# Performance work log

Hardware: AMD Instinct MI355X
Metric: run time of the kernel (lower is better)

## Reference

```python
import jax, jax.numpy as jnp
import numpy as np

B, C, H, W = 2, 256, 64, 64
HEADS, DIM_HEAD = 8, 64
INNER = HEADS * DIM_HEAD


def setup_inputs() -> dict:
    key = jax.random.key(0)
    k1, k2, k3, k4 = jax.random.split(key, 4)
    x = jax.random.normal(k1, (B, C, H, W), dtype=jnp.float32)
    # 1x1 conv weights stored as [out_ch, in_ch]
    w_qkv = jax.random.normal(k2, (3 * INNER, C), dtype=jnp.float32) * (1.0 / np.sqrt(C))
    w_out = jax.random.normal(k3, (C, INNER), dtype=jnp.float32) * (1.0 / np.sqrt(INNER))
    b_out = jax.random.normal(k4, (C,), dtype=jnp.float32) * 0.01
    return {"x": x, "w_qkv": w_qkv, "w_out": w_out, "b_out": b_out}


def reference(x, w_qkv, w_out, b_out):
    b, c, h, w = x.shape
    n = h * w
    # 1x1 conv == channel matmul
    qkv = jnp.einsum('oc,bchw->bohw', w_qkv, x)  # [B, 3*inner, H, W]
    qkv = qkv.reshape(b, 3, HEADS, DIM_HEAD, n)
    qkv = jnp.transpose(qkv, (1, 0, 2, 4, 3))    # [3, B, heads, N, dim_head]
    q, k, v = qkv[0], qkv[1], qkv[2]
    scale = 1.0 / (DIM_HEAD ** 0.5)
    dots = jnp.einsum('bhnd,bhmd->bhnm', q, k) * scale  # [B, heads, N, N]
    attn = jax.nn.softmax(dots, axis=-1)
    out = jnp.einsum('bhnm,bhmd->bhnd', attn, v)        # [B, heads, N, dim_head]
    out = jnp.transpose(out, (0, 1, 3, 2)).reshape(b, INNER, h, w)
    return jnp.einsum('ci,bihw->bchw', w_out, out) + b_out[None, :, None, None]
```

## Files before the change

kernel.cpp:

```cpp
#include <hip/hip_runtime.h>
#include <hip/hip_bf16.h>

typedef unsigned short u16;
typedef __attribute__((ext_vector_type(8))) short bf16x8;
typedef __attribute__((ext_vector_type(4))) float f32x4;
typedef __attribute__((ext_vector_type(8))) unsigned short u16x8;
typedef __attribute__((ext_vector_type(4))) unsigned short u16x4;

#define N_POS 4096
#define HEADS 8
#define DHEAD 64
#define CIN   256
#define INNER 512

__device__ __forceinline__ u16 f2bf(float f) {
    union { float f; unsigned int u; } v; v.f = f;
    unsigned int u = v.u + 0x7FFFu + ((v.u >> 16) & 1u);
    return (u16)(u >> 16);
}

__device__ __forceinline__ unsigned int pkbf2(float lo, float hi) {
    union { __hip_bfloat162 b; unsigned int u; } cv;
    cv.b = __float22bfloat162_rn(make_float2(lo, hi));
    return cv.u;
}

__global__ __launch_bounds__(256) void k0_prep(const float* __restrict__ x,
                                               const float* __restrict__ w_qkv,
                                               const float* __restrict__ w_out,
                                               u16* __restrict__ xT,
                                               u16* __restrict__ wq,
                                               u16* __restrict__ wo) {
    int bid = blockIdx.x;
    int t   = threadIdx.x;
    if (bid < 256) {
        int b = bid >> 7, rest = bid & 127;
        int n  = (rest & 15) * 256 + t;
        int c0 = (rest >> 4) * 32;
        const float* xp = x + (size_t)b * CIN * N_POS + n;
        u16* op = xT + ((size_t)(b * N_POS + n)) * CIN + c0;
        for (int g = 0; g < 4; ++g) {
            u16x8 v;
            for (int j = 0; j < 8; ++j)
                v[j] = f2bf(xp[(size_t)(c0 + g * 8 + j) * N_POS]);
            *(u16x8*)(op + g * 8) = v;
        }
    } else if (bid < 448) {
        size_t idx = (size_t)(bid - 256) * 2048 + t * 8;
        u16x8 v;
        for (int j = 0; j < 8; ++j) v[j] = f2bf(w_qkv[idx + j]);
        *(u16x8*)(wq + idx) = v;
    } else {
        size_t idx = (size_t)(bid - 448) * 2048 + t * 8;
        u16x8 v;
        for (int j = 0; j < 8; ++j) v[j] = f2bf(w_out[idx + j]);
        *(u16x8*)(wo + idx) = v;
    }
}

__global__ __launch_bounds__(256, 4) void k1_qkv(const u16* __restrict__ wq,
                                                 const u16* __restrict__ xT,
                                                 u16* __restrict__ q_ws,
                                                 u16* __restrict__ k_ws,
                                                 u16* __restrict__ vt_ws) {
    __shared__ u16 Alds[64 * 40];
    __shared__ u16 Blds[128 * 40];
    int tid = threadIdx.x;
    int n0  = blockIdx.x * 128;
    int by  = blockIdx.y;
    int b   = blockIdx.z;
    int o0  = by * 64;
    int sel = by >> 3;
    int h   = by & 7;
    int wv = tid >> 6, l = tid & 63, quad = l >> 4, l15 = l & 15;
    int srow = tid >> 2, sseg = tid & 3;
    int brow = tid >> 1, bseg = tid & 1;

    f32x4 acc[8] = {};
    for (int c0 = 0; c0 < CIN; c0 += 32) {
        *(u16x8*)&Alds[srow * 40 + sseg * 8] =
            *(const u16x8*)(wq + (size_t)(o0 + srow) * CIN + c0 + sseg * 8);
        const u16* xp = xT + ((size_t)(b * N_POS + n0 + brow)) * CIN + c0 + bseg * 16;
        *(u16x8*)&Blds[brow * 40 + bseg * 16]     = *(const u16x8*)xp;
        *(u16x8*)&Blds[brow * 40 + bseg * 16 + 8] = *(const u16x8*)(xp + 8);
        __syncthreads();
        bf16x8 af = *(const bf16x8*)&Alds[(wv * 16 + l15) * 40 + quad * 8];
        for (int nt = 0; nt < 8; ++nt) {
            bf16x8 bfrag = *(const bf16x8*)&Blds[(nt * 16 + l15) * 40 + quad * 8];
            acc[nt] = __builtin_amdgcn_mfma_f32_16x16x32_bf16(af, bfrag, acc[nt], 0, 0, 0);
        }
        __syncthreads();
    }
    const float QSCALE = 0.125f * 1.44269504088896f;
    float sc = (sel == 0) ? QSCALE : 1.0f;
    int dbase = wv * 16 + quad * 4;
    for (int nt = 0; nt < 8; ++nt) {
        int n = n0 + nt * 16 + l15;
        if (sel < 2) {
            u16* base = (sel == 0) ? q_ws : k_ws;
            u16x4 pk;
            for (int r = 0; r < 4; ++r) pk[r] = f2bf(acc[nt][r] * sc);
            *(u16x4*)&base[((size_t)((b * HEADS + h) * N_POS + n)) * DHEAD + dbase] = pk;
        } else {
            for (int r = 0; r < 4; ++r)
                vt_ws[((size_t)((b * HEADS + h) * DHEAD + dbase + r)) * N_POS + n] =
                    f2bf(acc[nt][r]);
        }
    }
}

__global__ __launch_bounds__(512, 4) void k2_attn(const u16* __restrict__ q_ws,
                                                  const u16* __restrict__ k_ws,
                                                  const u16* __restrict__ vt_ws,
                                                  u16* __restrict__ obf) {
    __shared__ u16 Klds[64 * 72];
    __shared__ u16 Vlds[64 * 72];
    int tid = threadIdx.x;
    int q0  = blockIdx.x * 256;
    int bh  = blockIdx.y;
    int wv = tid >> 6, l = tid & 63, quad = l >> 4, l15 = l & 15;
    int srow = tid >> 3, sseg = tid & 7;
    int srowp = (srow & 0x23) | ((srow & 4) << 2) | ((srow & 0x18) >> 1);

    const u16* qp = q_ws + ((size_t)(bh * N_POS + q0 + wv * 32 + l15)) * DHEAD + quad * 8;
    bf16x8 bq[2][2];
    for (int it = 0; it < 2; ++it) {
        bq[it][0] = *(const bf16x8*)(qp + (size_t)it * 16 * DHEAD);
        bq[it][1] = *(const bf16x8*)(qp + (size_t)it * 16 * DHEAD + 32);
    }

    f32x4 Oacc[2][4] = {};
    float lsum[2] = {0.f, 0.f};

    const u16* kp = k_ws + ((size_t)(bh * N_POS + srow)) * DHEAD + sseg * 8;
    const u16* vp = vt_ws + ((size_t)(bh * DHEAD + srow)) * N_POS + sseg * 8;

    u16x8 pf0 = *(const u16x8*)kp;
    u16x8 pf1 = *(const u16x8*)vp;

    for (int j0 = 0; j0 < N_POS; j0 += 64) {
        *(u16x8*)&Klds[srowp * 72 + sseg * 8] = pf0;
        *(u16x8*)&Vlds[srow * 72 + sseg * 8]  = pf1;
        __syncthreads();

        if (j0 + 64 < N_POS) {
            pf0 = *(const u16x8*)(kp + (size_t)(j0 + 64) * DHEAD);
            pf1 = *(const u16x8*)(vp + j0 + 64);
        }

        unsigned int pkw[2][2][4];
        for (int p = 0; p < 2; ++p)
            for (int a = 0; a < 2; ++a) {
                const u16* kb = &Klds[((2 * p + a) * 16 + l15) * 72 + quad * 8];
                bf16x8 kf0 = *(const bf16x8*)kb;
                bf16x8 kf1 = *(const bf16x8*)(kb + 32);
                f32x4 z[2];
                __builtin_amdgcn_s_setprio(1);
                for (int it = 0; it < 2; ++it) {
                    f32x4 t = {};
                    t = __builtin_amdgcn_mfma_f32_16x16x32_bf16(kf0, bq[it][0], t, 0, 0, 0);
                    t = __builtin_amdgcn_mfma_f32_16x16x32_bf16(kf1, bq[it][1], t, 0, 0, 0);
                    z[it] = t;
                }
                __builtin_amdgcn_s_setprio(0);
                for (int it = 0; it < 2; ++it) {
                    float e0 = __builtin_amdgcn_exp2f(z[it][0]);
                    float e1 = __builtin_amdgcn_exp2f(z[it][1]);
                    float e2 = __builtin_amdgcn_exp2f(z[it][2]);
                    float e3 = __builtin_amdgcn_exp2f(z[it][3]);
                    lsum[it] += (e0 + e1) + (e2 + e3);
                    pkw[it][p][2 * a]     = pkbf2(e0, e1);
                    pkw[it][p][2 * a + 1] = pkbf2(e2, e3);
                }
            }

        __builtin_amdgcn_s_setprio(1);
        for (int dt = 0; dt < 4; ++dt)
            for (int p = 0; p < 2; ++p) {
                bf16x8 vf = *(const bf16x8*)&Vlds[(dt * 16 + l15) * 72 + p * 32 + quad * 8];
                for (int it = 0; it < 2; ++it) {
                    union { unsigned int u[4]; bf16x8 v; } cv;
                    cv.u[0] = pkw[it][p][0]; cv.u[1] = pkw[it][p][1];
                    cv.u[2] = pkw[it][p][2]; cv.u[3] = pkw[it][p][3];
                    Oacc[it][dt] = __builtin_amdgcn_mfma_f32_16x16x32_bf16(vf, cv.v, Oacc[it][dt], 0, 0, 0);
                }
            }
        __builtin_amdgcn_s_setprio(0);
        __syncthreads();
    }

    int b = bh >> 3, h = bh & 7;
    for (int it = 0; it < 2; ++it) {
        float ls = lsum[it];
        ls += __shfl_xor(ls, 16);
        ls += __shfl_xor(ls, 32);
        float inv = 1.0f / ls;
        int n = q0 + wv * 32 + it * 16 + l15;
        u16* dst = obf + ((size_t)(b * N_POS + n)) * INNER + h * DHEAD;
        for (int dt = 0; dt < 4; ++dt) {
            u16x4 pk;
            for (int r = 0; r < 4; ++r) pk[r] = f2bf(Oacc[it][dt][r] * inv);
            *(u16x4*)&dst[dt * 16 + quad * 4] = pk;
        }
    }
}

__global__ __launch_bounds__(256) void k3_out(const u16* __restrict__ wo,
                                              const float* __restrict__ b_out,
                                              const u16* __restrict__ obf,
                                              float* __restrict__ out) {
    __shared__ u16 Alds[256 * 40];
    __shared__ u16 Blds[32 * 40];
    int tid = threadIdx.x;
    int n0 = blockIdx.x * 32;
    int b  = blockIdx.y;
    int wv = tid >> 6, l = tid & 63, quad = l >> 4, l15 = l & 15;

    f32x4 acc[4][2] = {};
    for (int i0 = 0; i0 < INNER; i0 += 32) {
        for (int rep = 0; rep < 4; ++rep) {
            int row = rep * 64 + (tid >> 2), seg = tid & 3;
            *(u16x8*)&Alds[row * 40 + seg * 8] =
                *(const u16x8*)(wo + (size_t)row * INNER + i0 + seg * 8);
        }
        if (tid < 128) {
            int srow = tid >> 2, sseg = tid & 3;
            *(u16x8*)&Blds[srow * 40 + sseg * 8] =
                *(const u16x8*)(obf + ((size_t)(b * N_POS + n0 + srow)) * INNER + i0 + sseg * 8);
        }
        __syncthreads();
        for (int ac = 0; ac < 4; ++ac) {
            bf16x8 af = *(const bf16x8*)&Alds[(wv * 64 + ac * 16 + l15) * 40 + quad * 8];
            for (int nt = 0; nt < 2; ++nt) {
                bf16x8 bfrag = *(const bf16x8*)&Blds[(nt * 16 + l15) * 40 + quad * 8];
                acc[ac][nt] = __builtin_amdgcn_mfma_f32_16x16x32_bf16(af, bfrag, acc[ac][nt], 0, 0, 0);
            }
        }
        __syncthreads();
    }
    for (int ac = 0; ac < 4; ++ac)
        for (int r = 0; r < 4; ++r) {
            int c = wv * 64 + ac * 16 + quad * 4 + r;
            float bias = b_out[c];
            for (int nt = 0; nt < 2; ++nt) {
                int n = n0 + nt * 16 + l15;
                out[((size_t)(b * CIN + c)) * N_POS + n] = acc[ac][nt][r] + bias;
            }
        }
}

extern "C" void kernel_launch(void* const* d_in, const int* in_sizes, int n_in,
                              void* d_out, int out_size, void* d_ws, size_t ws_size,
                              hipStream_t stream) {
    const float* x     = (const float*)d_in[0];
    const float* w_qkv = (const float*)d_in[1];
    const float* w_out = (const float*)d_in[2];
    const float* b_out = (const float*)d_in[3];
    float* out = (float*)d_out;

    u16* ws    = (u16*)d_ws;
    u16* xT    = ws;
    u16* q_ws  = xT   + (size_t)2 * N_POS * CIN;
    u16* k_ws  = q_ws + (size_t)2 * HEADS * N_POS * DHEAD;
    u16* vt_ws = k_ws + (size_t)2 * HEADS * N_POS * DHEAD;
    u16* wq_bf = vt_ws + (size_t)2 * HEADS * N_POS * DHEAD;
    u16* wo_bf = wq_bf + (size_t)3 * INNER * CIN;
    u16* obf   = wo_bf + (size_t)CIN * INNER;

    hipLaunchKernelGGL(k0_prep, dim3(512), dim3(256), 0, stream,
                       x, w_qkv, w_out, xT, wq_bf, wo_bf);
    hipLaunchKernelGGL(k1_qkv, dim3(32, 24, 2), dim3(256), 0, stream,
                       wq_bf, xT, q_ws, k_ws, vt_ws);
    hipLaunchKernelGGL(k2_attn, dim3(16, 16), dim3(512), 0, stream,
                       q_ws, k_ws, vt_ws, obf);
    hipLaunchKernelGGL(k3_out, dim3(128, 2), dim3(256), 0, stream,
                       wo_bf, b_out, obf, out);
}
```

Baseline: 189.0 us.

## Split attention over key chunks and double query tile per block

The attention kernel now splits the key range into four chunks along a new grid dimension. Each block covers 512 queries, so every wave handles 64 queries, which doubles K/V reuse per LDS load. Unnormalized partial outputs and row sums go to workspace, and the output projection sums the partials and normalizes them while loading its B tile. This cuts per-block K/V traffic and adds parallelism, at the cost of more registers per thread, extra partial-output memory traffic and extra bf16 rounding in the reduction.

```diff
diff --git a/kernel.cpp b/kernel.cpp
--- a/kernel.cpp
+++ b/kernel.cpp
@@ -12,11 +12,18 @@
 #define DHEAD 64
 #define CIN   256
 #define INNER 512
+#define NSPLIT 4
+#define JCHUNK (N_POS / NSPLIT)
 
 __device__ __forceinline__ u16 f2bf(float f) {
     union { float f; unsigned int u; } v; v.f = f;
     unsigned int u = v.u + 0x7FFFu + ((v.u >> 16) & 1u);
     return (u16)(u >> 16);
+}
+
+__device__ __forceinline__ float bf2f(u16 h) {
+    union { float f; unsigned int u; } v; v.u = ((unsigned int)h) << 16;
+    return v.f;
 }
 
 __device__ __forceinline__ unsigned int pkbf2(float lo, float hi) {
@@ -112,58 +119,61 @@
 __global__ __launch_bounds__(512, 4) void k2_attn(const u16* __restrict__ q_ws,
                                                   const u16* __restrict__ k_ws,
                                                   const u16* __restrict__ vt_ws,
-                                                  u16* __restrict__ obf) {
+                                                  u16* __restrict__ op_ws,
+                                                  float* __restrict__ lw_ws) {
     __shared__ u16 Klds[64 * 72];
     __shared__ u16 Vlds[64 * 72];
     int tid = threadIdx.x;
-    int q0  = blockIdx.x * 256;
+    int q0  = blockIdx.x * 512;
     int bh  = blockIdx.y;
+    int half = blockIdx.z;
+    int jbase = half * JCHUNK;
     int wv = tid >> 6, l = tid & 63, quad = l >> 4, l15 = l & 15;
     int srow = tid >> 3, sseg = tid & 7;
     int srowp = (srow & 0x23) | ((srow & 4) << 2) | ((srow & 0x18) >> 1);
 
-    const u16* qp = q_ws + ((size_t)(bh * N_POS + q0 + wv * 32 + l15)) * DHEAD + quad * 8;
-    bf16x8 bq[2][2];
-    for (int it = 0; it < 2; ++it) {
+    const u16* qp = q_ws + ((size_t)(bh * N_POS + q0 + wv * 64 + l15)) * DHEAD + quad * 8;
+    bf16x8 bq[4][2];
+    for (int it = 0; it < 4; ++it) {
         bq[it][0] = *(const bf16x8*)(qp + (size_t)it * 16 * DHEAD);
         bq[it][1] = *(const bf16x8*)(qp + (size_t)it * 16 * DHEAD + 32);
     }
 
-    f32x4 Oacc[2][4] = {};
-    float lsum[2] = {0.f, 0.f};
+    f32x4 Oacc[4][4] = {};
+    float lsum[4] = {0.f, 0.f, 0.f, 0.f};
 
     const u16* kp = k_ws + ((size_t)(bh * N_POS + srow)) * DHEAD + sseg * 8;
     const u16* vp = vt_ws + ((size_t)(bh * DHEAD + srow)) * N_POS + sseg * 8;
 
-    u16x8 pf0 = *(const u16x8*)kp;
-    u16x8 pf1 = *(const u16x8*)vp;
-
-    for (int j0 = 0; j0 < N_POS; j0 += 64) {
+    u16x8 pf0 = *(const u16x8*)(kp + (size_t)jbase * DHEAD);
+    u16x8 pf1 = *(const u16x8*)(vp + jbase);
+
+    for (int j0 = jbase; j0 < jbase + JCHUNK; j0 += 64) {
         *(u16x8*)&Klds[srowp * 72 + sseg * 8] = pf0;
         *(u16x8*)&Vlds[srow * 72 + sseg * 8]  = pf1;
         __syncthreads();
 
-        if (j0 + 64 < N_POS) {
+        if (j0 + 64 < jbase + JCHUNK) {
             pf0 = *(const u16x8*)(kp + (size_t)(j0 + 64) * DHEAD);
             pf1 = *(const u16x8*)(vp + j0 + 64);
         }
 
-        unsigned int pkw[2][2][4];
+        unsigned int pkw[4][2][4];
         for (int p = 0; p < 2; ++p)
             for (int a = 0; a < 2; ++a) {
                 const u16* kb = &Klds[((2 * p + a) * 16 + l15) * 72 + quad * 8];
                 bf16x8 kf0 = *(const bf16x8*)kb;
                 bf16x8 kf1 = *(const bf16x8*)(kb + 32);
-                f32x4 z[2];
+                f32x4 z[4];
                 __builtin_amdgcn_s_setprio(1);
-                for (int it = 0; it < 2; ++it) {
+                for (int it = 0; it < 4; ++it) {
                     f32x4 t = {};
                     t = __builtin_amdgcn_mfma_f32_16x16x32_bf16(kf0, bq[it][0], t, 0, 0, 0);
                     t = __builtin_amdgcn_mfma_f32_16x16x32_bf16(kf1, bq[it][1], t, 0, 0, 0);
                     z[it] = t;
                 }
                 __builtin_amdgcn_s_setprio(0);
-                for (int it = 0; it < 2; ++it) {
+                for (int it = 0; it < 4; ++it) {
                     float e0 = __builtin_amdgcn_exp2f(z[it][0]);
                     float e1 = __builtin_amdgcn_exp2f(z[it][1]);
                     float e2 = __builtin_amdgcn_exp2f(z[it][2]);
@@ -178,7 +188,7 @@
         for (int dt = 0; dt < 4; ++dt)
             for (int p = 0; p < 2; ++p) {
                 bf16x8 vf = *(const bf16x8*)&Vlds[(dt * 16 + l15) * 72 + p * 32 + quad * 8];
-                for (int it = 0; it < 2; ++it) {
+                for (int it = 0; it < 4; ++it) {
                     union { unsigned int u[4]; bf16x8 v; } cv;
                     cv.u[0] = pkw[it][p][0]; cv.u[1] = pkw[it][p][1];
                     cv.u[2] = pkw[it][p][2]; cv.u[3] = pkw[it][p][3];
@@ -190,16 +200,18 @@
     }
 
     int b = bh >> 3, h = bh & 7;
-    for (int it = 0; it < 2; ++it) {
+    u16* opb = op_ws + (size_t)half * 2 * N_POS * INNER;
+    float* lwb = lw_ws + (size_t)half * 2 * HEADS * N_POS;
+    for (int it = 0; it < 4; ++it) {
         float ls = lsum[it];
         ls += __shfl_xor(ls, 16);
         ls += __shfl_xor(ls, 32);
-        float inv = 1.0f / ls;
-        int n = q0 + wv * 32 + it * 16 + l15;
-        u16* dst = obf + ((size_t)(b * N_POS + n)) * INNER + h * DHEAD;
+        int n = q0 + wv * 64 + it * 16 + l15;
+        if (quad == 0) lwb[(size_t)bh * N_POS + n] = ls;
+        u16* dst = opb + ((size_t)(b * N_POS + n)) * INNER + h * DHEAD;
         for (int dt = 0; dt < 4; ++dt) {
             u16x4 pk;
-            for (int r = 0; r < 4; ++r) pk[r] = f2bf(Oacc[it][dt][r] * inv);
+            for (int r = 0; r < 4; ++r) pk[r] = f2bf(Oacc[it][dt][r]);
             *(u16x4*)&dst[dt * 16 + quad * 4] = pk;
         }
     }
@@ -207,7 +219,8 @@
 
 __global__ __launch_bounds__(256) void k3_out(const u16* __restrict__ wo,
                                               const float* __restrict__ b_out,
-                                              const u16* __restrict__ obf,
+                                              const u16* __restrict__ op_ws,
+                                              const float* __restrict__ lw_ws,
                                               float* __restrict__ out) {
     __shared__ u16 Alds[256 * 40];
     __shared__ u16 Blds[32 * 40];
@@ -225,8 +238,23 @@
         }
         if (tid < 128) {
             int srow = tid >> 2, sseg = tid & 3;
-            *(u16x8*)&Blds[srow * 40 + sseg * 8] =
-                *(const u16x8*)(obf + ((size_t)(b * N_POS + n0 + srow)) * INNER + i0 + sseg * 8);
+            int i = i0 + sseg * 8;
+            int h = i >> 6;
+            int n = n0 + srow;
+            size_t lidx = ((size_t)(b * HEADS + h)) * N_POS + n;
+            float ls = 0.f;
+            for (int hf = 0; hf < NSPLIT; ++hf)
+                ls += lw_ws[(size_t)hf * 2 * HEADS * N_POS + lidx];
+            float inv = 1.0f / ls;
+            size_t oidx = ((size_t)(b * N_POS + n)) * INNER + i;
+            float s[8] = {};
+            for (int hf = 0; hf < NSPLIT; ++hf) {
+                u16x8 pv = *(const u16x8*)(op_ws + (size_t)hf * 2 * N_POS * INNER + oidx);
+                for (int k = 0; k < 8; ++k) s[k] += bf2f(pv[k]);
+            }
+            u16x8 v;
+            for (int k = 0; k < 8; ++k) v[k] = f2bf(s[k] * inv);
+            *(u16x8*)&Blds[srow * 40 + sseg * 8] = v;
         }
         __syncthreads();
         for (int ac = 0; ac < 4; ++ac) {
@@ -265,14 +293,15 @@
     u16* vt_ws = k_ws + (size_t)2 * HEADS * N_POS * DHEAD;
     u16* wq_bf = vt_ws + (size_t)2 * HEADS * N_POS * DHEAD;
     u16* wo_bf = wq_bf + (size_t)3 * INNER * CIN;
-    u16* obf   = wo_bf + (size_t)CIN * INNER;
+    u16* op_ws = wo_bf + (size_t)CIN * INNER;
+    float* lw_ws = (float*)(op_ws + (size_t)NSPLIT * 2 * N_POS * INNER);
 
     hipLaunchKernelGGL(k0_prep, dim3(512), dim3(256), 0, stream,
                        x, w_qkv, w_out, xT, wq_bf, wo_bf);
     hipLaunchKernelGGL(k1_qkv, dim3(32, 24, 2), dim3(256), 0, stream,
                        wq_bf, xT, q_ws, k_ws, vt_ws);
-    hipLaunchKernelGGL(k2_attn, dim3(16, 16), dim3(512), 0, stream,
-                       q_ws, k_ws, vt_ws, obf);
+    hipLaunchKernelGGL(k2_attn, dim3(8, 16, NSPLIT), dim3(512), 0, stream,
+                       q_ws, k_ws, vt_ws, op_ws, lw_ws);
     hipLaunchKernelGGL(k3_out, dim3(128, 2), dim3(256), 0, stream,
-                       wo_bf, b_out, obf, out);
-}
+                       wo_bf, b_out, op_ws, lw_ws, out);
+}
```

Result: slower. 440.1 us (+132.8%).
